# Performance work log

Hardware: AMD Instinct MI355X
Metric: run time of the kernel (lower is better)

The kernel has to match this reference:

```python
import jax, jax.numpy as jnp
import numpy as np

N, E, IN_DIM, HID, TOWERS, NG = 20000, 320000, 16, 50, 5, 64
FO = HID // TOWERS  # out channels per tower = 10
EPS_BN = 1e-5
EPS_STD = 1e-5  # PyG StdAggregation: sqrt(relu(var) + 1e-5)


def setup_inputs() -> dict:
    key = jax.random.key(0)
    ks = jax.random.split(key, 24)
    rn = lambda k, shape: jax.random.normal(k, shape, dtype=jnp.float32) * 0.1
    F0, F1 = IN_DIM, HID
    return {
        "x": jax.random.normal(ks[0], (N, IN_DIM), dtype=jnp.float32),
        "edge_index": jax.random.randint(ks[1], (2, E), 0, N),
        "batch": jnp.sort(jax.random.randint(ks[2], (N,), 0, NG)),
        # conv0: pre Linear(2*F0 -> F0) per tower, post Linear(13*F0 -> FO) per tower, lin Linear(HID->HID)
        "pre_W0": rn(ks[3], (TOWERS, F0, 2 * F0)), "pre_b0": rn(ks[4], (TOWERS, F0)),
        "post_W0": rn(ks[5], (TOWERS, FO, 13 * F0)), "post_b0": rn(ks[6], (TOWERS, FO)),
        "lin_W0": rn(ks[7], (HID, HID)), "lin_b0": rn(ks[8], (HID,)),
        "gamma0": jnp.ones((HID,), jnp.float32), "beta0": jnp.zeros((HID,), jnp.float32),
        # conv1
        "pre_W1": rn(ks[9], (TOWERS, F1, 2 * F1)), "pre_b1": rn(ks[10], (TOWERS, F1)),
        "post_W1": rn(ks[11], (TOWERS, FO, 13 * F1)), "post_b1": rn(ks[12], (TOWERS, FO)),
        "lin_W1": rn(ks[13], (HID, HID)), "lin_b1": rn(ks[14], (HID,)),
        "gamma1": jnp.ones((HID,), jnp.float32), "beta1": jnp.zeros((HID,), jnp.float32),
        # head MLP: HID->50->25->1
        "mlp_W1": rn(ks[15], (50, HID)), "mlp_b1": rn(ks[16], (50,)),
        "mlp_W2": rn(ks[17], (25, 50)), "mlp_b2": rn(ks[18], (25,)),
        "mlp_W3": rn(ks[19], (1, 25)), "mlp_b3": rn(ks[20], (1,)),
    }


def pna_conv(x, src, dst, deg, avg_log, pre_W, pre_b, post_W, post_b, lin_W, lin_b):
    # x: [N, F]; divide_input=False -> every tower sees the full F features.
    n, Fi = x.shape
    T = pre_W.shape[0]
    # message: h = cat([x_i, x_j]) = cat([x[dst], x[src]]), then per-tower pre-MLP (1 Linear)
    h = jnp.concatenate([x[dst], x[src]], axis=-1)                  # [E, 2F]
    hs = jnp.einsum('ef,tgf->etg', h, pre_W) + pre_b                # [E, T, F]
    flat = hs.reshape(hs.shape[0], T * Fi)                          # [E, T*F]
    # multi-aggregation: mean / min / max / std, scattered to dst
    s = jax.ops.segment_sum(flat, dst, num_segments=n)
    s2 = jax.ops.segment_sum(flat * flat, dst, num_segments=n)
    mn = jax.ops.segment_min(flat, dst, num_segments=n)
    mx = jax.ops.segment_max(flat, dst, num_segments=n)
    degc = jnp.maximum(deg, 1.0)[:, None]
    mean = s / degc
    var = s2 / degc - mean * mean
    std = jnp.sqrt(jax.nn.relu(var) + EPS_STD)
    has = (deg > 0)[:, None]
    mn = jnp.where(has, mn, 0.0)
    mx = jnp.where(has, mx, 0.0)
    agg = jnp.concatenate([mean.reshape(n, T, Fi), mn.reshape(n, T, Fi),
                           mx.reshape(n, T, Fi), std.reshape(n, T, Fi)], axis=-1)  # [N,T,4F]
    # degree scalers: identity, amplification, attenuation
    amp = (jnp.log(jnp.maximum(deg, 1.0) + 1.0) / avg_log)[:, None, None]
    out = jnp.concatenate([jnp.broadcast_to(x[:, None, :], (n, T, Fi)),
                           agg, agg * amp, agg / amp], axis=-1)      # [N, T, 13F]
    out = jnp.einsum('ntf,tgf->ntg', out, post_W) + post_b          # [N, T, FO]
    return out.reshape(n, T * post_W.shape[1]) @ lin_W.T + lin_b    # [N, HID]


def _bn_relu(h, g, b):
    mu = h.mean(axis=0)
    v = jnp.mean((h - mu) ** 2, axis=0)  # biased var, torch BN training-mode normalization
    return jax.nn.relu(g * (h - mu) / jnp.sqrt(v + EPS_BN) + b)


def reference(x, edge_index, batch,
              pre_W0, pre_b0, post_W0, post_b0, lin_W0, lin_b0, gamma0, beta0,
              pre_W1, pre_b1, post_W1, post_b1, lin_W1, lin_b1, gamma1, beta1,
              mlp_W1, mlp_b1, mlp_W2, mlp_b2, mlp_W3, mlp_b3):
    src, dst = edge_index[0], edge_index[1]
    n = x.shape[0]
    deg = jax.ops.segment_sum(jnp.ones((src.shape[0],), jnp.float32), dst, num_segments=n)
    avg_log = jnp.mean(jnp.log(deg + 1.0))  # PNA avg_deg['log'] from this graph's degree histogram
    # NOTE: zip(convs, batch_norms) in the torch forward applies only num_conv_layer=2 convs.
    h = pna_conv(x, src, dst, deg, avg_log, pre_W0, pre_b0, post_W0, post_b0, lin_W0, lin_b0)
    h = _bn_relu(h, gamma0, beta0)
    h = pna_conv(h, src, dst, deg, avg_log, pre_W1, pre_b1, post_W1, post_b1, lin_W1, lin_b1)
    h = _bn_relu(h, gamma1, beta1)
    cnt = jax.ops.segment_sum(jnp.ones((n,), jnp.float32), batch, num_segments=NG)
    pooled = jax.ops.segment_sum(h, batch, num_segments=NG) / jnp.maximum(cnt, 1.0)[:, None]
    h = jax.nn.relu(pooled @ mlp_W1.T + mlp_b1)
    h = jax.nn.relu(h @ mlp_W2.T + mlp_b2)
    return h @ mlp_W3.T + mlp_b3  # [NG, 1]
```

## Files before the change

kernel.cpp:

```cpp
#include <hip/hip_runtime.h>
#include <math.h>
#include <float.h>

#define NN 20000
#define EE 320000
#define INDIM 16
#define HID 50
#define TW 5
#define FO 10
#define NGROUPS 64
#define NBINS 64
#define NBLK 2556

typedef float f4 __attribute__((ext_vector_type(4)));
typedef float f2 __attribute__((ext_vector_type(2)));
typedef _Float16 h4 __attribute__((ext_vector_type(4)));

__device__ inline f4 f4_min(f4 a, f4 b) {
    f4 r; r.x = fminf(a.x, b.x); r.y = fminf(a.y, b.y);
    r.z = fminf(a.z, b.z); r.w = fminf(a.w, b.w); return r;
}
__device__ inline f4 f4_max(f4 a, f4 b) {
    f4 r; r.x = fmaxf(a.x, b.x); r.y = fmaxf(a.y, b.y);
    r.z = fmaxf(a.z, b.z); r.w = fmaxf(a.w, b.w); return r;
}
__device__ inline f4 h2f(h4 h) {
    f4 r; r.x = (float)h.x; r.y = (float)h.y; r.z = (float)h.z; r.w = (float)h.w; return r;
}
__device__ inline float sh3sum(float v, int g0, int G_) {
    return v + __shfl(v, g0 + G_, 64) + __shfl(v, g0 + 2 * G_, 64);
}
__device__ inline float sh3min(float v, int g0, int G_) {
    return fminf(fminf(v, __shfl(v, g0 + G_, 64)), __shfl(v, g0 + 2 * G_, 64));
}
__device__ inline float sh3max(float v, int g0, int G_) {
    return fmaxf(fmaxf(v, __shfl(v, g0 + G_, 64)), __shfl(v, g0 + 2 * G_, 64));
}
__device__ inline void acc4(float& acc, f4 w, float a0, float a1, float a2, float a3) {
    acc += w.x * a0; acc += w.y * a1; acc += w.z * a2; acc += w.w * a3;
}

__global__ void k_deg(const int* __restrict__ dst, int* __restrict__ deg) {
    int e = blockIdx.x * 256 + threadIdx.x;
    if (e < EE) atomicAdd(&deg[dst[e]], 1);
}

__global__ void k_scan(const int* __restrict__ deg, int* __restrict__ offsets,
                       float* __restrict__ scal, int* __restrict__ padStart) {
    __shared__ int part[1024];
    __shared__ float fred[1024];
    __shared__ int lhist[NBINS];
    const int CH = 20;
    int tid = threadIdx.x;
    if (tid < NBINS) lhist[tid] = 0;
    __syncthreads();
    int base = tid * CH;
    int loc[CH];
    int s = 0; float fs = 0.f;
    for (int c = 0; c < CH; ++c) {
        int idx = base + c;
        int v = (idx < NN) ? deg[idx] : 0;
        loc[c] = s; s += v;
        if (idx < NN) {
            fs += logf((float)v + 1.0f);
            atomicAdd(&lhist[min(v, NBINS - 1)], 1);
        }
    }
    part[tid] = s; fred[tid] = fs; __syncthreads();
    for (int off = 1; off < 1024; off <<= 1) {
        int v = (tid >= off) ? part[tid - off] : 0;
        __syncthreads();
        part[tid] += v;
        __syncthreads();
    }
    int pre = (tid > 0) ? part[tid - 1] : 0;
    for (int c = 0; c < CH; ++c) {
        int idx = base + c;
        if (idx < NN) offsets[idx] = pre + loc[c];
    }
    if (tid == 0) offsets[NN] = part[1023];
    for (int off = 512; off > 0; off >>= 1) {
        if (tid < off) fred[tid] += fred[tid + off];
        __syncthreads();
    }
    if (tid == 0) {
        scal[0] = fred[0] / (float)NN;
        int acc = 0;
        for (int b = 0; b < NBINS; ++b) {
            padStart[b] = acc;
            acc += (lhist[b] + 7) & ~7;
        }
        padStart[NBINS] = acc;
    }
}

__global__ void k_fill(const int* __restrict__ src, const int* __restrict__ dst,
                       const int* __restrict__ offsets, int* __restrict__ cursor,
                       int* __restrict__ csr_src) {
    int e = blockIdx.x * 256 + threadIdx.x;
    if (e < EE) {
        int d = dst[e];
        int pos = offsets[d] + atomicAdd(&cursor[d], 1);
        csr_src[pos] = src[e];
    }
}

__global__ void k_scatter(const int* __restrict__ deg, const int* __restrict__ padStart,
                          int* __restrict__ binCur, int* __restrict__ nodeList,
                          int* __restrict__ slotBin) {
    int i = blockIdx.x * 256 + threadIdx.x;
    if (i < NN) {
        int bin = min(deg[i], NBINS - 1);
        int pos = padStart[bin] + atomicAdd(&binCur[bin], 1);
        nodeList[pos] = i;
        slotBin[pos] = bin;
    }
}

__global__ void k_wprime(const float* __restrict__ postW0, const float* __restrict__ postW1,
                         const float* __restrict__ scal,
                         float* __restrict__ Wp0, float* __restrict__ Wp1) {
    int bin = blockIdx.y;
    float degf = fmaxf((float)bin, 1.f);
    float amp = logf(degf + 1.f) / scal[0];
    float ia = 1.f / amp;
    int x = blockIdx.x, t = threadIdx.x;
    int k = t >> 2, j = t & 3;
    if (x < 65) {
        int sq = x;
        int seg = sq / 13, q = sq % 13, f = q * 4 + j;
        float v = 0.f;
        if (f < 50 && k < 50) {
            if (seg == 0) v = postW1[k * 650 + f];
            else {
                int s = seg - 1;
                v = postW1[k * 650 + (1 + s) * 50 + f]
                  + amp * postW1[k * 650 + (5 + s) * 50 + f]
                  + ia * postW1[k * 650 + (9 + s) * 50 + f];
            }
        }
        Wp1[((size_t)bin * 65 + sq) * 256 + t] = v;
    } else {
        int sq = x - 65;
        int seg, f;
        if (sq < 4) { seg = 0; f = sq * 4 + j; }
        else { seg = 1 + (sq - 4) / 4; f = ((sq - 4) % 4) * 4 + j; }
        float v = 0.f;
        if (k < 50) {
            if (seg == 0) v = postW0[k * 208 + f];
            else {
                int s = seg - 1;
                v = postW0[k * 208 + (1 + s) * 16 + f]
                  + amp * postW0[k * 208 + (5 + s) * 16 + f]
                  + ia * postW0[k * 208 + (9 + s) * 16 + f];
            }
        }
        Wp0[((size_t)bin * 20 + sq) * 256 + t] = v;
    }
}

__global__ void k_pack(const float* __restrict__ preW0, const float* __restrict__ preW1,
                       const float* __restrict__ linW0, const float* __restrict__ linW1,
                       float* __restrict__ preWt0, float* __restrict__ preWt1,
                       float* __restrict__ Lt0, float* __restrict__ Lt1) {
    int idx = blockIdx.x * 256 + threadIdx.x;
    int job = blockIdx.y;
    int q = idx >> 8, k = (idx >> 2) & 63, j = idx & 3;
    switch (job) {
    case 0:
        if (idx < 32 * 80) { int c = idx / 80, r = idx % 80; preWt0[idx] = preW0[r * 32 + c]; }
        break;
    case 1:
        if (idx < 100 * 256) { int c = idx / 256, r = idx % 256; preWt1[idx] = (r < 250) ? preW1[r * 100 + c] : 0.f; }
        break;
    case 2:
        if (idx < 13 * 256) { int f = q * 4 + j; Lt0[idx] = (f < 50 && k < HID) ? linW0[k * 50 + f] : 0.f; }
        break;
    case 3:
        if (idx < 13 * 256) { int f = q * 4 + j; Lt1[idx] = (f < 50 && k < HID) ? linW1[k * 50 + f] : 0.f; }
        break;
    }
}

template <int F, int TF, int TFP, bool BN>
__global__ __launch_bounds__(256, 4) void k_gemm_CP(
    const float* __restrict__ x, const float* __restrict__ preWt,
    const float* __restrict__ b,
    const float* __restrict__ bnacc, const float* __restrict__ gam,
    const float* __restrict__ bet,
    float* __restrict__ C, _Float16* __restrict__ P) {
    const int NODES = 16;
    __shared__ float xs[NODES * F];
    int tid = threadIdx.x;
    int base = blockIdx.x * NODES;
    for (int idx = tid; idx < NODES * F; idx += 256) {
        float v = x[(size_t)base * F + idx];
        if (BN) {
            int c = idx % F;
            float mu = bnacc[c] * (1.f / NN);
            float var = bnacc[64 + c] * (1.f / NN) - mu * mu;
            v = fmaxf(gam[c] * (v - mu) * rsqrtf(var + 1e-5f) + bet[c], 0.f);
        }
        xs[idx] = v;
    }
    __syncthreads();
    if (tid < TF) {
        float accC[NODES], accP[NODES];
#pragma unroll
        for (int n = 0; n < NODES; ++n) { accC[n] = 0.f; accP[n] = 0.f; }
        for (int f = 0; f < F; ++f) {
            float wl = preWt[f * TFP + tid];
            float wr = preWt[(F + f) * TFP + tid];
#pragma unroll
            for (int n = 0; n < NODES; ++n) {
                float xv = xs[n * F + f];
                accC[n] += xv * wl;
                accP[n] += xv * wr;
            }
        }
        float bb = b[tid];
        for (int n = 0; n < NODES; ++n) {
            C[((size_t)(base + n)) * TFP + tid] = accC[n] + bb;
            P[((size_t)(base + n)) * TFP + tid] = (_Float16)accP[n];
        }
    } else if (tid < TFP) {
        for (int n = 0; n < NODES; ++n) {
            C[((size_t)(base + n)) * TFP + tid] = 0.f;
            P[((size_t)(base + n)) * TFP + tid] = (_Float16)0.f;
        }
    }
}

template <int F, int TFPG, int TFPL, int EP, int SQ, int SQX, bool AF4, bool BNIN>
__global__ __launch_bounds__(256, 4) void k_conv(
    const float* __restrict__ xin, const float* __restrict__ C, const _Float16* __restrict__ P,
    const int* __restrict__ offsets, const int* __restrict__ csr,
    const int* __restrict__ nodeList, const int* __restrict__ slotBin,
    const float* __restrict__ Wp,
    const float* __restrict__ postb, const float* __restrict__ Lt,
    const float* __restrict__ linb,
    const float* __restrict__ bn_in, const float* __restrict__ g_in,
    const float* __restrict__ b_in,
    float* __restrict__ hout, float* __restrict__ bn_out) {
    const int GP = TFPG / 4;
    const int GL = TFPL / 4;
    const int WQ = SQX + 4 * SQ;
    __shared__ __align__(16) float sAgg[8][4][TFPL];
    __shared__ __align__(16) float sX[8][SQX * 4];
    __shared__ __align__(16) float sY[8][52];
    __shared__ float sBN[4][2][64];
    int t = threadIdx.x, w = t >> 6, lane = t & 63;
    int sbase = blockIdx.x * 8;
    int nodeId[2];

    for (int nn = 0; nn < 2; ++nn) {
        int nd = 2 * w + nn;
        int i = nodeList[sbase + nd];
        nodeId[nn] = i;
        if (i < 0) continue;
        int beg = offsets[i], end = offsets[i + 1];
        int d = end - beg;
        int g = (EP == 1) ? lane : (lane % GL);
        int e = (EP == 1) ? 0 : (lane / GL);
        bool act = (EP == 1) ? (lane < GL) : (e < EP);
        f4 S = {0.f, 0.f, 0.f, 0.f}, S2 = {0.f, 0.f, 0.f, 0.f};
        f4 MN = {FLT_MAX, FLT_MAX, FLT_MAX, FLT_MAX};
        f4 MX = {-FLT_MAX, -FLT_MAX, -FLT_MAX, -FLT_MAX};
        const h4* __restrict__ Pv = (const h4*)P;
        if (act) {
            if (EP == 1) {
                int j = beg;
                for (; j + 4 <= end; j += 4) {
                    int s0 = csr[j], s1 = csr[j + 1], s2 = csr[j + 2], s3 = csr[j + 3];
                    f4 a = h2f(Pv[(size_t)s0 * GP + g]);
                    f4 b = h2f(Pv[(size_t)s1 * GP + g]);
                    f4 c = h2f(Pv[(size_t)s2 * GP + g]);
                    f4 dd = h2f(Pv[(size_t)s3 * GP + g]);
                    S += a; S2 += a * a; MN = f4_min(MN, a); MX = f4_max(MX, a);
                    S += b; S2 += b * b; MN = f4_min(MN, b); MX = f4_max(MX, b);
                    S += c; S2 += c * c; MN = f4_min(MN, c); MX = f4_max(MX, c);
                    S += dd; S2 += dd * dd; MN = f4_min(MN, dd); MX = f4_max(MX, dd);
                }
                for (; j < end; ++j) {
                    int s0 = csr[j];
                    f4 a = h2f(Pv[(size_t)s0 * GP + g]);
                    S += a; S2 += a * a; MN = f4_min(MN, a); MX = f4_max(MX, a);
                }
            } else {
                int j = beg + e;
                for (; j + EP < end; j += 2 * EP) {
                    int s0 = csr[j], s1 = csr[j + EP];
                    f4 a = h2f(Pv[(size_t)s0 * GP + g]);
                    f4 b = h2f(Pv[(size_t)s1 * GP + g]);
                    S += a; S2 += a * a; MN = f4_min(MN, a); MX = f4_max(MX, a);
                    S += b; S2 += b * b; MN = f4_min(MN, b); MX = f4_max(MX, b);
                }
                if (j < end) {
                    int s0 = csr[j];
                    f4 a = h2f(Pv[(size_t)s0 * GP + g]);
                    S += a; S2 += a * a; MN = f4_min(MN, a); MX = f4_max(MX, a);
                }
            }
        }
        if (EP == 3) {
            int g0 = lane % GL;
            S.x = sh3sum(S.x, g0, GL); S.y = sh3sum(S.y, g0, GL);
            S.z = sh3sum(S.z, g0, GL); S.w = sh3sum(S.w, g0, GL);
            S2.x = sh3sum(S2.x, g0, GL); S2.y = sh3sum(S2.y, g0, GL);
            S2.z = sh3sum(S2.z, g0, GL); S2.w = sh3sum(S2.w, g0, GL);
            MN.x = sh3min(MN.x, g0, GL); MN.y = sh3min(MN.y, g0, GL);
            MN.z = sh3min(MN.z, g0, GL); MN.w = sh3min(MN.w, g0, GL);
            MX.x = sh3max(MX.x, g0, GL); MX.y = sh3max(MX.y, g0, GL);
            MX.z = sh3max(MX.z, g0, GL); MX.w = sh3max(MX.w, g0, GL);
        }
        if (lane < GL) {
            f4 Cv = ((const f4*)C)[(size_t)i * GP + lane];
            float degf = (float)d;
            float rdegc = 1.0f / fmaxf(degf, 1.0f);
            f4 mean, sq, var, stdv, mnv, mxv;
            mean.x = (degf * Cv.x + S.x) * rdegc; mean.y = (degf * Cv.y + S.y) * rdegc;
            mean.z = (degf * Cv.z + S.z) * rdegc; mean.w = (degf * Cv.w + S.w) * rdegc;
            sq.x = degf * Cv.x * Cv.x + 2.f * Cv.x * S.x + S2.x;
            sq.y = degf * Cv.y * Cv.y + 2.f * Cv.y * S.y + S2.y;
            sq.z = degf * Cv.z * Cv.z + 2.f * Cv.z * S.z + S2.z;
            sq.w = degf * Cv.w * Cv.w + 2.f * Cv.w * S.w + S2.w;
            var.x = sq.x * rdegc - mean.x * mean.x; var.y = sq.y * rdegc - mean.y * mean.y;
            var.z = sq.z * rdegc - mean.z * mean.z; var.w = sq.w * rdegc - mean.w * mean.w;
            stdv.x = sqrtf(fmaxf(var.x, 0.f) + 1e-5f); stdv.y = sqrtf(fmaxf(var.y, 0.f) + 1e-5f);
            stdv.z = sqrtf(fmaxf(var.z, 0.f) + 1e-5f); stdv.w = sqrtf(fmaxf(var.w, 0.f) + 1e-5f);
            if (d > 0) {
                mnv.x = Cv.x + MN.x; mnv.y = Cv.y + MN.y; mnv.z = Cv.z + MN.z; mnv.w = Cv.w + MN.w;
                mxv.x = Cv.x + MX.x; mxv.y = Cv.y + MX.y; mxv.z = Cv.z + MX.z; mxv.w = Cv.w + MX.w;
            } else {
                mnv = (f4){0.f, 0.f, 0.f, 0.f}; mxv = mnv;
            }
            ((f4*)&sAgg[nd][0][0])[lane] = mean;
            ((f4*)&sAgg[nd][1][0])[lane] = mnv;
            ((f4*)&sAgg[nd][2][0])[lane] = mxv;
            ((f4*)&sAgg[nd][3][0])[lane] = stdv;
        }
        if (BNIN) {
            if (lane < F) {
                float hv = xin[(size_t)i * F + lane];
                float mu = bn_in[lane] * (1.f / NN);
                float var = bn_in[64 + lane] * (1.f / NN) - mu * mu;
                sX[nd][lane] = fmaxf(g_in[lane] * (hv - mu) * rsqrtf(var + 1e-5f) + b_in[lane], 0.f);
            } else if (lane < SQX * 4) {
                sX[nd][lane] = 0.f;
            }
        } else {
            if (lane < F) sX[nd][lane] = xin[(size_t)i * F + lane];
            else if (lane < SQX * 4) sX[nd][lane] = 0.f;
        }
    }
    int bin = slotBin[sbase];
    const f4* __restrict__ Wv = (const f4*)(Wp + (size_t)bin * WQ * 256);
    __syncthreads();

    int nd0 = 2 * w, nd1 = 2 * w + 1;
    int kk = (lane < HID) ? lane : (HID - 1);
    int tw = kk / FO;
    float ya = 0.f, yb = 0.f;
#pragma unroll
    for (int q = 0; q < SQX; ++q) {
        f4 wv = Wv[q * 64 + lane];
        f4 a0 = *(const f4*)(&sX[nd0][4 * q]);
        f4 a1 = *(const f4*)(&sX[nd1][4 * q]);
        acc4(ya, wv, a0.x, a0.y, a0.z, a0.w);
        acc4(yb, wv, a1.x, a1.y, a1.z, a1.w);
    }
#pragma unroll
    for (int s = 0; s < 4; ++s) {
        const float* __restrict__ A0 = &sAgg[nd0][s][tw * F];
        const float* __restrict__ A1 = &sAgg[nd1][s][tw * F];
#pragma unroll 4
        for (int q = 0; q < SQ; ++q) {
            f4 wv = Wv[(SQX + s * SQ + q) * 64 + lane];
            float a00, a01, a02, a03, a10, a11, a12, a13;
            if constexpr (AF4) {
                f4 v0 = *(const f4*)(A0 + 4 * q);
                f4 v1 = *(const f4*)(A1 + 4 * q);
                a00 = v0.x; a01 = v0.y; a02 = v0.z; a03 = v0.w;
                a10 = v1.x; a11 = v1.y; a12 = v1.z; a13 = v1.w;
            } else {
                f2 p0 = *(const f2*)(A0 + 4 * q);
                f2 p1 = *(const f2*)(A0 + 4 * q + 2);
                f2 q0 = *(const f2*)(A1 + 4 * q);
                f2 q1 = *(const f2*)(A1 + 4 * q + 2);
                a00 = p0.x; a01 = p0.y; a02 = p1.x; a03 = p1.y;
                a10 = q0.x; a11 = q0.y; a12 = q1.x; a13 = q1.y;
            }
            acc4(ya, wv, a00, a01, a02, a03);
            acc4(yb, wv, a10, a11, a12, a13);
        }
    }
    float pb = postb[kk];
    ya += pb; yb += pb;
    if (lane < HID) { sY[nd0][lane] = ya; sY[nd1][lane] = yb; }
    else if (lane < 52) { sY[nd0][lane] = 0.f; sY[nd1][lane] = 0.f; }

    const f4* __restrict__ Lv = (const f4*)Lt;
    float lb = linb[kk];
    float oa = lb, ob = lb;
#pragma unroll
    for (int q = 0; q < 13; ++q) {
        f4 lv = Lv[q * 64 + lane];
        f4 s0 = *(const f4*)(&sY[nd0][4 * q]);
        f4 s1 = *(const f4*)(&sY[nd1][4 * q]);
        acc4(oa, lv, s0.x, s0.y, s0.z, s0.w);
        acc4(ob, lv, s1.x, s1.y, s1.z, s1.w);
    }
    if (lane < HID) {
        if (nodeId[0] >= 0) hout[(size_t)nodeId[0] * HID + lane] = oa;
        if (nodeId[1] >= 0) hout[(size_t)nodeId[1] * HID + lane] = ob;
    }

    float sv = 0.f, sv2 = 0.f;
    if (lane < HID) {
        if (nodeId[0] >= 0) { sv += oa; sv2 += oa * oa; }
        if (nodeId[1] >= 0) { sv += ob; sv2 += ob * ob; }
    }
    sBN[w][0][lane] = sv;
    sBN[w][1][lane] = sv2;
    __syncthreads();
    if (t < 64 && lane < HID) {
        float s = sBN[0][0][lane] + sBN[1][0][lane] + sBN[2][0][lane] + sBN[3][0][lane];
        float s2 = sBN[0][1][lane] + sBN[1][1][lane] + sBN[2][1][lane] + sBN[3][1][lane];
        atomicAdd(&bn_out[lane], s);
        atomicAdd(&bn_out[64 + lane], s2);
    }
}

__global__ void k_head(const float* __restrict__ h, const int* __restrict__ batch,
                       const float* __restrict__ bnacc, const float* __restrict__ gam,
                       const float* __restrict__ bet,
                       const float* __restrict__ W1, const float* __restrict__ b1,
                       const float* __restrict__ W2, const float* __restrict__ b2,
                       const float* __restrict__ W3, const float* __restrict__ b3,
                       float* __restrict__ out) {
    __shared__ float sp[HID], h1[50], h2[25];
    __shared__ int sbound[2];
    int g = blockIdx.x, tid = threadIdx.x;
    if (tid < 2) {
        int target = g + tid;
        int lo = 0, hi = NN;
        while (lo < hi) {
            int mid = (lo + hi) >> 1;
            if (batch[mid] < target) lo = mid + 1; else hi = mid;
        }
        sbound[tid] = lo;
    }
    __syncthreads();
    int beg = sbound[0], end = sbound[1];
    if (tid < HID) {
        float mu = bnacc[tid] * (1.f / NN);
        float var = bnacc[64 + tid] * (1.f / NN) - mu * mu;
        float sc = gam[tid] * rsqrtf(var + 1e-5f);
        float sh = bet[tid] - mu * sc;
        float s0 = 0.f, s1 = 0.f, s2 = 0.f, s3 = 0.f;
        int n = beg;
        for (; n + 4 <= end; n += 4) {
            s0 += fmaxf(fmaf(h[(size_t)n * HID + tid], sc, sh), 0.f);
            s1 += fmaxf(fmaf(h[(size_t)(n + 1) * HID + tid], sc, sh), 0.f);
            s2 += fmaxf(fmaf(h[(size_t)(n + 2) * HID + tid], sc, sh), 0.f);
            s3 += fmaxf(fmaf(h[(size_t)(n + 3) * HID + tid], sc, sh), 0.f);
        }
        for (; n < end; ++n) s0 += fmaxf(fmaf(h[(size_t)n * HID + tid], sc, sh), 0.f);
        sp[tid] = (s0 + s1 + s2 + s3) / fmaxf((float)(end - beg), 1.0f);
    }
    __syncthreads();
    if (tid < 50) {
        float a = b1[tid];
        for (int k = 0; k < HID; ++k) a += W1[tid * HID + k] * sp[k];
        h1[tid] = fmaxf(a, 0.f);
    }
    __syncthreads();
    if (tid < 25) {
        float a = b2[tid];
        for (int k = 0; k < 50; ++k) a += W2[tid * 50 + k] * h1[k];
        h2[tid] = fmaxf(a, 0.f);
    }
    __syncthreads();
    if (tid == 0) {
        float a = b3[0];
        for (int k = 0; k < 25; ++k) a += W3[k] * h2[k];
        out[g] = a;
    }
}

extern "C" void kernel_launch(void* const* d_in, const int* in_sizes, int n_in,
                              void* d_out, int out_size, void* d_ws, size_t ws_size,
                              hipStream_t stream) {
    const float* x      = (const float*)d_in[0];
    const int*   ei     = (const int*)d_in[1];
    const int*   batch  = (const int*)d_in[2];
    const float* preW0  = (const float*)d_in[3];
    const float* preb0  = (const float*)d_in[4];
    const float* postW0 = (const float*)d_in[5];
    const float* postb0 = (const float*)d_in[6];
    const float* linW0  = (const float*)d_in[7];
    const float* linb0  = (const float*)d_in[8];
    const float* gamma0 = (const float*)d_in[9];
    const float* beta0  = (const float*)d_in[10];
    const float* preW1  = (const float*)d_in[11];
    const float* preb1  = (const float*)d_in[12];
    const float* postW1 = (const float*)d_in[13];
    const float* postb1 = (const float*)d_in[14];
    const float* linW1  = (const float*)d_in[15];
    const float* linb1  = (const float*)d_in[16];
    const float* gamma1 = (const float*)d_in[17];
    const float* beta1  = (const float*)d_in[18];
    const float* mW1    = (const float*)d_in[19];
    const float* mb1    = (const float*)d_in[20];
    const float* mW2    = (const float*)d_in[21];
    const float* mb2    = (const float*)d_in[22];
    const float* mW3    = (const float*)d_in[23];
    const float* mb3    = (const float*)d_in[24];
    float* out = (float*)d_out;
    (void)in_sizes; (void)n_in; (void)out_size; (void)ws_size;

    char* ws = (char*)d_ws;
    size_t off = 0;
    auto alloc = [&](size_t bytes) -> void* {
        void* p = ws + off;
        off += (bytes + 255) & ~(size_t)255;
        return p;
    };
    int*   deg     = (int*)alloc((size_t)NN * 4);
    int*   cursor  = (int*)alloc((size_t)NN * 4);
    float* bnacc0  = (float*)alloc(128 * 4);
    float* bnacc1  = (float*)alloc(128 * 4);
    int*   binCur  = (int*)alloc(NBINS * 4);
    int*   slotBin = (int*)alloc((size_t)(NBLK * 8) * 4);
    size_t zero_bytes = off;
    int*   nodeList = (int*)alloc((size_t)(NBLK * 8) * 4);
    int*   padStart = (int*)alloc((NBINS + 1) * 4);
    int*   offsets = (int*)alloc((size_t)(NN + 1) * 4);
    int*   csr_src = (int*)alloc((size_t)EE * 4);
    float* scal    = (float*)alloc(64);
    float* preWt0  = (float*)alloc((size_t)32 * 80 * 4);
    float* preWt1  = (float*)alloc((size_t)100 * 256 * 4);
    float* Lt0     = (float*)alloc((size_t)13 * 256 * 4);
    float* Lt1     = (float*)alloc((size_t)13 * 256 * 4);
    float* Wp0     = (float*)alloc((size_t)NBINS * 20 * 256 * 4);
    float* Wp1     = (float*)alloc((size_t)NBINS * 65 * 256 * 4);
    float* Cbuf    = (float*)alloc((size_t)NN * 256 * 4);
    _Float16* Pbuf = (_Float16*)alloc((size_t)NN * 256 * 2);
    float* h1buf   = (float*)alloc((size_t)NN * HID * 4);
    float* h2buf   = (float*)alloc((size_t)NN * HID * 4);

    const int* src = ei;
    const int* dst = ei + EE;

    hipMemsetAsync(ws, 0, zero_bytes, stream);
    hipMemsetAsync(nodeList, 0xFF, (size_t)(NBLK * 8) * 4, stream);

    k_pack<<<dim3(100, 4), 256, 0, stream>>>(preW0, preW1, linW0, linW1,
                                             preWt0, preWt1, Lt0, Lt1);
    k_deg<<<EE / 256, 256, 0, stream>>>(dst, deg);
    k_scan<<<1, 1024, 0, stream>>>(deg, offsets, scal, padStart);
    k_fill<<<EE / 256, 256, 0, stream>>>(src, dst, offsets, cursor, csr_src);
    k_scatter<<<(NN + 255) / 256, 256, 0, stream>>>(deg, padStart, binCur, nodeList, slotBin);
    k_wprime<<<dim3(85, NBINS), 256, 0, stream>>>(postW0, postW1, scal, Wp0, Wp1);

    k_gemm_CP<INDIM, 80, 80, false><<<NN / 16, 256, 0, stream>>>(
        x, preWt0, preb0, nullptr, nullptr, nullptr, Cbuf, Pbuf);
    k_conv<INDIM, 80, 80, 3, 4, 4, true, false><<<NBLK, 256, 0, stream>>>(
        x, Cbuf, Pbuf, offsets, csr_src, nodeList, slotBin, Wp0, postb0, Lt0, linb0,
        nullptr, nullptr, nullptr, h1buf, bnacc0);

    k_gemm_CP<HID, 250, 256, true><<<NN / 16, 256, 0, stream>>>(
        h1buf, preWt1, preb1, bnacc0, gamma0, beta0, Cbuf, Pbuf);
    k_conv<HID, 256, 252, 1, 13, 13, false, true><<<NBLK, 256, 0, stream>>>(
        h1buf, Cbuf, Pbuf, offsets, csr_src, nodeList, slotBin, Wp1, postb1, Lt1, linb1,
        bnacc0, gamma0, beta0, h2buf, bnacc1);

    k_head<<<NGROUPS, 64, 0, stream>>>(h2buf, batch, bnacc1, gamma1, beta1,
                                       mW1, mb1, mW2, mb2, mW3, mb3, out);
}
```

Measured before the change: 366.3 us.

## Fold degree binning into scan, drop slotBin, enlarge GEMM tiles, unroll gathers

```diff
diff --git a/kernel.cpp b/kernel.cpp
--- a/kernel.cpp
+++ b/kernel.cpp
@@ -39,6 +39,7 @@
 __device__ inline void acc4(float& acc, f4 w, float a0, float a1, float a2, float a3) {
     acc += w.x * a0; acc += w.y * a1; acc += w.z * a2; acc += w.w * a3;
 }
+#define STAT(a) { S += (a); S2 += (a) * (a); MN = f4_min(MN, (a)); MX = f4_max(MX, (a)); }
 
 __global__ void k_deg(const int* __restrict__ dst, int* __restrict__ deg) {
     int e = blockIdx.x * 256 + threadIdx.x;
@@ -46,13 +47,15 @@
 }
 
 __global__ void k_scan(const int* __restrict__ deg, int* __restrict__ offsets,
-                       float* __restrict__ scal, int* __restrict__ padStart) {
+                       float* __restrict__ scal, int* __restrict__ nodeList) {
     __shared__ int part[1024];
     __shared__ float fred[1024];
     __shared__ int lhist[NBINS];
+    __shared__ int spad[NBINS];
+    __shared__ int lcur[NBINS];
     const int CH = 20;
     int tid = threadIdx.x;
-    if (tid < NBINS) lhist[tid] = 0;
+    if (tid < NBINS) { lhist[tid] = 0; lcur[tid] = 0; }
     __syncthreads();
     int base = tid * CH;
     int loc[CH];
@@ -87,10 +90,18 @@
         scal[0] = fred[0] / (float)NN;
         int acc = 0;
         for (int b = 0; b < NBINS; ++b) {
-            padStart[b] = acc;
+            spad[b] = acc;
             acc += (lhist[b] + 7) & ~7;
         }
-        padStart[NBINS] = acc;
+    }
+    __syncthreads();
+    for (int c = 0; c < CH; ++c) {
+        int idx = base + c;
+        if (idx < NN) {
+            int bin = min(deg[idx], NBINS - 1);
+            int pos = spad[bin] + atomicAdd(&lcur[bin], 1);
+            nodeList[pos] = idx;
+        }
     }
 }
 
@@ -102,18 +113,6 @@
         int d = dst[e];
         int pos = offsets[d] + atomicAdd(&cursor[d], 1);
         csr_src[pos] = src[e];
-    }
-}
-
-__global__ void k_scatter(const int* __restrict__ deg, const int* __restrict__ padStart,
-                          int* __restrict__ binCur, int* __restrict__ nodeList,
-                          int* __restrict__ slotBin) {
-    int i = blockIdx.x * 256 + threadIdx.x;
-    if (i < NN) {
-        int bin = min(deg[i], NBINS - 1);
-        int pos = padStart[bin] + atomicAdd(&binCur[bin], 1);
-        nodeList[pos] = i;
-        slotBin[pos] = bin;
     }
 }
 
@@ -182,14 +181,13 @@
     }
 }
 
-template <int F, int TF, int TFP, bool BN>
-__global__ __launch_bounds__(256, 4) void k_gemm_CP(
+template <int F, int TF, int TFP, int NODES, bool BN>
+__global__ __launch_bounds__(256, 2) void k_gemm_CP(
     const float* __restrict__ x, const float* __restrict__ preWt,
     const float* __restrict__ b,
     const float* __restrict__ bnacc, const float* __restrict__ gam,
     const float* __restrict__ bet,
     float* __restrict__ C, _Float16* __restrict__ P) {
-    const int NODES = 16;
     __shared__ float xs[NODES * F];
     int tid = threadIdx.x;
     int base = blockIdx.x * NODES;
@@ -219,11 +217,13 @@
             }
         }
         float bb = b[tid];
+#pragma unroll
         for (int n = 0; n < NODES; ++n) {
             C[((size_t)(base + n)) * TFP + tid] = accC[n] + bb;
             P[((size_t)(base + n)) * TFP + tid] = (_Float16)accP[n];
         }
     } else if (tid < TFP) {
+#pragma unroll
         for (int n = 0; n < NODES; ++n) {
             C[((size_t)(base + n)) * TFP + tid] = 0.f;
             P[((size_t)(base + n)) * TFP + tid] = (_Float16)0.f;
@@ -235,7 +235,7 @@
 __global__ __launch_bounds__(256, 4) void k_conv(
     const float* __restrict__ xin, const float* __restrict__ C, const _Float16* __restrict__ P,
     const int* __restrict__ offsets, const int* __restrict__ csr,
-    const int* __restrict__ nodeList, const int* __restrict__ slotBin,
+    const int* __restrict__ nodeList, const int* __restrict__ deg,
     const float* __restrict__ Wp,
     const float* __restrict__ postb, const float* __restrict__ Lt,
     const float* __restrict__ linb,
@@ -270,35 +270,47 @@
         if (act) {
             if (EP == 1) {
                 int j = beg;
+                for (; j + 8 <= end; j += 8) {
+                    int s0 = csr[j], s1 = csr[j + 1], s2 = csr[j + 2], s3 = csr[j + 3];
+                    int s4 = csr[j + 4], s5 = csr[j + 5], s6 = csr[j + 6], s7 = csr[j + 7];
+                    f4 a0 = h2f(Pv[(size_t)s0 * GP + g]);
+                    f4 a1 = h2f(Pv[(size_t)s1 * GP + g]);
+                    f4 a2 = h2f(Pv[(size_t)s2 * GP + g]);
+                    f4 a3 = h2f(Pv[(size_t)s3 * GP + g]);
+                    f4 a4 = h2f(Pv[(size_t)s4 * GP + g]);
+                    f4 a5 = h2f(Pv[(size_t)s5 * GP + g]);
+                    f4 a6 = h2f(Pv[(size_t)s6 * GP + g]);
+                    f4 a7 = h2f(Pv[(size_t)s7 * GP + g]);
+                    STAT(a0) STAT(a1) STAT(a2) STAT(a3)
+                    STAT(a4) STAT(a5) STAT(a6) STAT(a7)
+                }
                 for (; j + 4 <= end; j += 4) {
                     int s0 = csr[j], s1 = csr[j + 1], s2 = csr[j + 2], s3 = csr[j + 3];
-                    f4 a = h2f(Pv[(size_t)s0 * GP + g]);
-                    f4 b = h2f(Pv[(size_t)s1 * GP + g]);
-                    f4 c = h2f(Pv[(size_t)s2 * GP + g]);
-                    f4 dd = h2f(Pv[(size_t)s3 * GP + g]);
-                    S += a; S2 += a * a; MN = f4_min(MN, a); MX = f4_max(MX, a);
-                    S += b; S2 += b * b; MN = f4_min(MN, b); MX = f4_max(MX, b);
-                    S += c; S2 += c * c; MN = f4_min(MN, c); MX = f4_max(MX, c);
-                    S += dd; S2 += dd * dd; MN = f4_min(MN, dd); MX = f4_max(MX, dd);
+                    f4 a0 = h2f(Pv[(size_t)s0 * GP + g]);
+                    f4 a1 = h2f(Pv[(size_t)s1 * GP + g]);
+                    f4 a2 = h2f(Pv[(size_t)s2 * GP + g]);
+                    f4 a3 = h2f(Pv[(size_t)s3 * GP + g]);
+                    STAT(a0) STAT(a1) STAT(a2) STAT(a3)
                 }
                 for (; j < end; ++j) {
                     int s0 = csr[j];
-                    f4 a = h2f(Pv[(size_t)s0 * GP + g]);
-                    S += a; S2 += a * a; MN = f4_min(MN, a); MX = f4_max(MX, a);
+                    f4 a0 = h2f(Pv[(size_t)s0 * GP + g]);
+                    STAT(a0)
                 }
             } else {
                 int j = beg + e;
-                for (; j + EP < end; j += 2 * EP) {
-                    int s0 = csr[j], s1 = csr[j + EP];
-                    f4 a = h2f(Pv[(size_t)s0 * GP + g]);
-                    f4 b = h2f(Pv[(size_t)s1 * GP + g]);
-                    S += a; S2 += a * a; MN = f4_min(MN, a); MX = f4_max(MX, a);
-                    S += b; S2 += b * b; MN = f4_min(MN, b); MX = f4_max(MX, b);
+                for (; j + 3 * EP < end; j += 4 * EP) {
+                    int s0 = csr[j], s1 = csr[j + EP], s2 = csr[j + 2 * EP], s3 = csr[j + 3 * EP];
+                    f4 a0 = h2f(Pv[(size_t)s0 * GP + g]);
+                    f4 a1 = h2f(Pv[(size_t)s1 * GP + g]);
+                    f4 a2 = h2f(Pv[(size_t)s2 * GP + g]);
+                    f4 a3 = h2f(Pv[(size_t)s3 * GP + g]);
+                    STAT(a0) STAT(a1) STAT(a2) STAT(a3)
                 }
-                if (j < end) {
+                for (; j < end; j += EP) {
                     int s0 = csr[j];
-                    f4 a = h2f(Pv[(size_t)s0 * GP + g]);
-                    S += a; S2 += a * a; MN = f4_min(MN, a); MX = f4_max(MX, a);
+                    f4 a0 = h2f(Pv[(size_t)s0 * GP + g]);
+                    STAT(a0)
                 }
             }
         }
@@ -353,7 +365,8 @@
             else if (lane < SQX * 4) sX[nd][lane] = 0.f;
         }
     }
-    int bin = slotBin[sbase];
+    int fn = nodeList[sbase];
+    int bin = (fn >= 0) ? min(deg[fn], NBINS - 1) : 0;
     const f4* __restrict__ Wv = (const f4*)(Wp + (size_t)bin * WQ * 256);
     __syncthreads();
 
@@ -530,11 +543,8 @@
     int*   cursor  = (int*)alloc((size_t)NN * 4);
     float* bnacc0  = (float*)alloc(128 * 4);
     float* bnacc1  = (float*)alloc(128 * 4);
-    int*   binCur  = (int*)alloc(NBINS * 4);
-    int*   slotBin = (int*)alloc((size_t)(NBLK * 8) * 4);
     size_t zero_bytes = off;
     int*   nodeList = (int*)alloc((size_t)(NBLK * 8) * 4);
-    int*   padStart = (int*)alloc((NBINS + 1) * 4);
     int*   offsets = (int*)alloc((size_t)(NN + 1) * 4);
     int*   csr_src = (int*)alloc((size_t)EE * 4);
     float* scal    = (float*)alloc(64);
@@ -558,21 +568,20 @@
     k_pack<<<dim3(100, 4), 256, 0, stream>>>(preW0, preW1, linW0, linW1,
                                              preWt0, preWt1, Lt0, Lt1);
     k_deg<<<EE / 256, 256, 0, stream>>>(dst, deg);
-    k_scan<<<1, 1024, 0, stream>>>(deg, offsets, scal, padStart);
+    k_scan<<<1, 1024, 0, stream>>>(deg, offsets, scal, nodeList);
     k_fill<<<EE / 256, 256, 0, stream>>>(src, dst, offsets, cursor, csr_src);
-    k_scatter<<<(NN + 255) / 256, 256, 0, stream>>>(deg, padStart, binCur, nodeList, slotBin);
     k_wprime<<<dim3(85, NBINS), 256, 0, stream>>>(postW0, postW1, scal, Wp0, Wp1);
 
-    k_gemm_CP<INDIM, 80, 80, false><<<NN / 16, 256, 0, stream>>>(
+    k_gemm_CP<INDIM, 80, 80, 32, false><<<NN / 32, 256, 0, stream>>>(
         x, preWt0, preb0, nullptr, nullptr, nullptr, Cbuf, Pbuf);
     k_conv<INDIM, 80, 80, 3, 4, 4, true, false><<<NBLK, 256, 0, stream>>>(
-        x, Cbuf, Pbuf, offsets, csr_src, nodeList, slotBin, Wp0, postb0, Lt0, linb0,
+        x, Cbuf, Pbuf, offsets, csr_src, nodeList, deg, Wp0, postb0, Lt0, linb0,
         nullptr, nullptr, nullptr, h1buf, bnacc0);
 
-    k_gemm_CP<HID, 250, 256, true><<<NN / 16, 256, 0, stream>>>(
+    k_gemm_CP<HID, 250, 256, 32, true><<<NN / 32, 256, 0, stream>>>(
         h1buf, preWt1, preb1, bnacc0, gamma0, beta0, Cbuf, Pbuf);
     k_conv<HID, 256, 252, 1, 13, 13, false, true><<<NBLK, 256, 0, stream>>>(
-        h1buf, Cbuf, Pbuf, offsets, csr_src, nodeList, slotBin, Wp1, postb1, Lt1, linb1,
+        h1buf, Cbuf, Pbuf, offsets, csr_src, nodeList, deg, Wp1, postb1, Lt1, linb1,
         bnacc0, gamma0, beta0, h2buf, bnacc1);
 
     k_head<<<NGROUPS, 64, 0, stream>>>(h2buf, batch, bnacc1, gamma1, beta1,
```

New measurement: 325.9 us. 1.12x faster.
